# Optimization experiments

Hardware: AMD Instinct MI355X
Metric: run time of the kernel (lower is better)

The kernel has to match this reference:

```python
import jax, jax.numpy as jnp
import numpy as np

GREEDY_EPS = 1e-6

def setup_inputs() -> dict:
    key = jax.random.key(0)
    k1, k2, k3 = jax.random.split(key, 3)
    B, V = 256, 128000
    logits = jax.random.normal(k1, (B, V), dtype=jnp.float32)
    temperatures = jax.random.uniform(k2, (B,), dtype=jnp.float32)  # in (0,1); some rows near 0 -> greedy-ish
    u = jax.random.uniform(k3, (B, V), dtype=jnp.float32, minval=1e-10, maxval=1.0)
    return {"logits": logits, "temperatures": temperatures, "u": u}

def reference(logits, temperatures, u):
    # Greedy token per row
    greedy = jnp.argmax(logits, axis=-1)  # [B]
    # Temperature-scaled logits; guard temp<=eps rows against div-by-zero
    safe_t = jnp.where(temperatures <= GREEDY_EPS, 1.0, temperatures)  # [B]
    scaled = logits / safe_t[:, None]  # [B, V]
    # Gumbel-max trick: argmax(scaled + g), g ~ Gumbel(0,1), equals
    # multinomial sample from softmax(scaled) in distribution.
    gumbel = -jnp.log(-jnp.log(u))  # [B, V]
    sampled = jnp.argmax(scaled + gumbel, axis=-1)  # [B]
    # Per-row greedy fallback for temp <= eps (matches the torch loop)
    return jnp.where(temperatures <= GREEDY_EPS, greedy, sampled)
```

## Files before the change

### kernel.cpp

```cpp
#include <hip/hip_runtime.h>
#include <math.h>

#define GREEDY_EPS 1e-6f

__global__ __launch_bounds__(1024) void sampler_kernel(
    const float* __restrict__ logits,
    const float* __restrict__ temps,
    const float* __restrict__ u,
    int* __restrict__ out,
    int V)
{
    const int row = blockIdx.x;
    const int tid = threadIdx.x;
    const float t = temps[row];
    const bool greedy = (t <= GREEDY_EPS);

    const float4* __restrict__ lg4 =
        (const float4*)(logits + (size_t)row * (size_t)V);
    const float4* __restrict__ uu4 =
        (const float4*)(u + (size_t)row * (size_t)V);
    const int nvec = V >> 2;

    float bestVal = -INFINITY;
    int bestIdx = 0;

    if (greedy) {
        for (int i = tid; i < nvec; i += blockDim.x) {
            float4 l = lg4[i];
            int base = i << 2;
            if (l.x > bestVal) { bestVal = l.x; bestIdx = base; }
            if (l.y > bestVal) { bestVal = l.y; bestIdx = base + 1; }
            if (l.z > bestVal) { bestVal = l.z; bestIdx = base + 2; }
            if (l.w > bestVal) { bestVal = l.w; bestIdx = base + 3; }
        }
    } else {
        for (int i = tid; i < nvec; i += blockDim.x) {
            float4 l = lg4[i];
            float4 g = uu4[i];
            int base = i << 2;
            float v0 = l.x / t - logf(-logf(g.x));
            float v1 = l.y / t - logf(-logf(g.y));
            float v2 = l.z / t - logf(-logf(g.z));
            float v3 = l.w / t - logf(-logf(g.w));
            if (v0 > bestVal) { bestVal = v0; bestIdx = base; }
            if (v1 > bestVal) { bestVal = v1; bestIdx = base + 1; }
            if (v2 > bestVal) { bestVal = v2; bestIdx = base + 2; }
            if (v3 > bestVal) { bestVal = v3; bestIdx = base + 3; }
        }
    }

    const int lane = tid & 63;
    const int wave = tid >> 6;
    #pragma unroll
    for (int off = 32; off > 0; off >>= 1) {
        float ov = __shfl_down(bestVal, off);
        int   oi = __shfl_down(bestIdx, off);
        if (ov > bestVal || (ov == bestVal && oi < bestIdx)) {
            bestVal = ov; bestIdx = oi;
        }
    }

    __shared__ float sVal[16];
    __shared__ int   sIdx[16];
    if (lane == 0) { sVal[wave] = bestVal; sIdx[wave] = bestIdx; }
    __syncthreads();

    if (tid == 0) {
        float bv = sVal[0]; int bi = sIdx[0];
        const int nw = (int)(blockDim.x >> 6);
        for (int w = 1; w < nw; ++w) {
            float v = sVal[w]; int ix = sIdx[w];
            if (v > bv || (v == bv && ix < bi)) { bv = v; bi = ix; }
        }
        out[row] = bi;
    }
}

extern "C" void kernel_launch(void* const* d_in, const int* in_sizes, int n_in,
                              void* d_out, int out_size, void* d_ws, size_t ws_size,
                              hipStream_t stream) {
    const float* logits = (const float*)d_in[0];
    const float* temps  = (const float*)d_in[1];
    const float* u      = (const float*)d_in[2];
    int* out = (int*)d_out;

    const int B = in_sizes[1];
    const int V = in_sizes[0] / B;

    sampler_kernel<<<dim3(B), dim3(1024), 0, stream>>>(logits, temps, u, out, V);
}
```

Before: 50.90 us.

## Split each row across two blocks and use fast log2 Gumbel math

Each row is now split into two segments handled by separate blocks. Each block writes a packed (ordered float key, inverted index) partial to workspace, and a second small kernel takes the max to pick the winner. This doubles the grid from 256 to 512 blocks so more of the GPU is busy. The Gumbel computation also swaps logf and division for __log2f intrinsics with one FMA per element, scaling by temperature instead of dividing. That changes the rounding of the compared values, and an extra kernel launch is added.

Measured after the change: 47.02 us. 7.6% less time.

```diff
diff --git a/kernel.cpp b/kernel.cpp
--- a/kernel.cpp
+++ b/kernel.cpp
@@ -2,30 +2,42 @@
 #include <math.h>
 
 #define GREEDY_EPS 1e-6f
+#define SEG 2
+#define BLK 1024
 
-__global__ __launch_bounds__(1024) void sampler_kernel(
+__device__ inline unsigned int fkey(float v) {
+    unsigned int b = __float_as_uint(v);
+    return (b & 0x80000000u) ? ~b : (b | 0x80000000u);
+}
+
+__global__ __launch_bounds__(BLK) void sampler_partial(
     const float* __restrict__ logits,
     const float* __restrict__ temps,
     const float* __restrict__ u,
-    int* __restrict__ out,
+    unsigned long long* __restrict__ ws,
     int V)
 {
-    const int row = blockIdx.x;
+    const int row = blockIdx.x >> 1;
+    const int seg = blockIdx.x & 1;
     const int tid = threadIdx.x;
+
+    const int segLen = V / SEG;
+    const int segOff = seg * segLen;
+    const int nvec   = segLen >> 2;
+
     const float t = temps[row];
     const bool greedy = (t <= GREEDY_EPS);
 
     const float4* __restrict__ lg4 =
-        (const float4*)(logits + (size_t)row * (size_t)V);
+        (const float4*)(logits + (size_t)row * (size_t)V + segOff);
     const float4* __restrict__ uu4 =
-        (const float4*)(u + (size_t)row * (size_t)V);
-    const int nvec = V >> 2;
+        (const float4*)(u + (size_t)row * (size_t)V + segOff);
 
     float bestVal = -INFINITY;
     int bestIdx = 0;
 
     if (greedy) {
-        for (int i = tid; i < nvec; i += blockDim.x) {
+        for (int i = tid; i < nvec; i += BLK) {
             float4 l = lg4[i];
             int base = i << 2;
             if (l.x > bestVal) { bestVal = l.x; bestIdx = base; }
@@ -34,14 +46,20 @@
             if (l.w > bestVal) { bestVal = l.w; bestIdx = base + 3; }
         }
     } else {
-        for (int i = tid; i < nvec; i += blockDim.x) {
+        const float a   = -t * 0.69314718055994530942f;
+        const float ac1 = a * -0.52876637294489770425f;
+        for (int i = tid; i < nvec; i += BLK) {
             float4 l = lg4[i];
             float4 g = uu4[i];
             int base = i << 2;
-            float v0 = l.x / t - logf(-logf(g.x));
-            float v1 = l.y / t - logf(-logf(g.y));
-            float v2 = l.z / t - logf(-logf(g.z));
-            float v3 = l.w / t - logf(-logf(g.w));
+            float G0 = __log2f(-__log2f(g.x));
+            float G1 = __log2f(-__log2f(g.y));
+            float G2 = __log2f(-__log2f(g.z));
+            float G3 = __log2f(-__log2f(g.w));
+            float v0 = fmaf(a, G0, l.x + ac1);
+            float v1 = fmaf(a, G1, l.y + ac1);
+            float v2 = fmaf(a, G2, l.z + ac1);
+            float v3 = fmaf(a, G3, l.w + ac1);
             if (v0 > bestVal) { bestVal = v0; bestIdx = base; }
             if (v1 > bestVal) { bestVal = v1; bestIdx = base + 1; }
             if (v2 > bestVal) { bestVal = v2; bestIdx = base + 2; }
@@ -60,19 +78,38 @@
         }
     }
 
-    __shared__ float sVal[16];
-    __shared__ int   sIdx[16];
+    __shared__ float sVal[BLK / 64];
+    __shared__ int   sIdx[BLK / 64];
     if (lane == 0) { sVal[wave] = bestVal; sIdx[wave] = bestIdx; }
     __syncthreads();
 
     if (tid == 0) {
         float bv = sVal[0]; int bi = sIdx[0];
-        const int nw = (int)(blockDim.x >> 6);
-        for (int w = 1; w < nw; ++w) {
+        #pragma unroll
+        for (int w = 1; w < BLK / 64; ++w) {
             float v = sVal[w]; int ix = sIdx[w];
             if (v > bv || (v == bv && ix < bi)) { bv = v; bi = ix; }
         }
-        out[row] = bi;
+        int gidx = bi + segOff;
+        unsigned long long packed =
+            ((unsigned long long)fkey(bv) << 32) |
+            (unsigned long long)(0xFFFFFFFFu - (unsigned int)gidx);
+        ws[(size_t)row * SEG + seg] = packed;
+    }
+}
+
+__global__ void sampler_final(const unsigned long long* __restrict__ ws,
+                              int* __restrict__ out, int B)
+{
+    int row = blockIdx.x * blockDim.x + threadIdx.x;
+    if (row < B) {
+        unsigned long long m = ws[(size_t)row * SEG];
+        #pragma unroll
+        for (int s = 1; s < SEG; ++s) {
+            unsigned long long v = ws[(size_t)row * SEG + s];
+            if (v > m) m = v;
+        }
+        out[row] = (int)(0xFFFFFFFFu - (unsigned int)(m & 0xFFFFFFFFu));
     }
 }
 
@@ -87,5 +124,9 @@
     const int B = in_sizes[1];
     const int V = in_sizes[0] / B;
 
-    sampler_kernel<<<dim3(B), dim3(1024), 0, stream>>>(logits, temps, u, out, V);
+    unsigned long long* ws = (unsigned long long*)d_ws;
+
+    sampler_partial<<<dim3(B * SEG), dim3(BLK), 0, stream>>>(
+        logits, temps, u, ws, V);
+    sampler_final<<<dim3((B + 255) / 256), dim3(256), 0, stream>>>(ws, out, B);
 }
```
